# Kernel optimization log

Hardware: AMD Instinct MI355X
Metric: run time of the kernel (lower is better)

The kernel has to match this reference:

```python
import jax, jax.numpy as jnp
import numpy as np

B, NL, L1, D = 16, 12, 197, 768   # batch, num_layers, 1+num_patches, embed_dim
E, K, C, IMG = 4, 3, 21, 224      # num_experts, topk, num_classes, image_size


def setup_inputs() -> dict:
    key = jax.random.key(0)
    k0, k1, k2 = jax.random.split(key, 3)
    features = jax.random.normal(k0, (B, NL, L1, D), jnp.float32)
    gate_W = jax.random.normal(k1, (D, E), jnp.float32) / np.sqrt(D).astype(np.float32)
    gate_b = jnp.zeros((E,), jnp.float32)
    expert_W = jax.random.normal(k2, (E, D, C), jnp.float32) / np.sqrt(D).astype(np.float32)
    expert_b = jnp.zeros((E, C), jnp.float32)
    return dict(features=features, gate_W=gate_W, gate_b=gate_b,
                expert_W=expert_W, expert_b=expert_b)


def reference(features, gate_W, gate_b, expert_W, expert_b):
    cls_tokens = features[:, :, 0, :]          # [B, NL, D]
    feats = features[:, :, 1:, :]              # [B, NL, L, D]
    gate_score = cls_tokens @ gate_W + gate_b  # [B, NL, E]
    gate_prob = jax.nn.softmax(gate_score.transpose(0, 2, 1), axis=-1)  # [B, E, NL]
    # per-expert topk over layers (vectorized over experts)
    topv, topi = jax.lax.top_k(gate_prob, K)   # [B, E, K]
    # gather selected layer feature maps: [B, E, K, L, D]
    gathered = jnp.take_along_axis(feats[:, None], topi[:, :, :, None, None], axis=2)
    w = jax.nn.softmax(topv, axis=-1)          # re-softmax of topk values, [B, E, K]
    mixed = jnp.einsum('bek,bekld->beld', w, gathered)  # [B, E, L, D]
    # expert heads (UPerNet modeled as linear decode + bilinear upsample)
    logits = jnp.einsum('beld,edc->belc', mixed, expert_W) + expert_b[None, :, None, :]
    L = logits.shape[2]
    g = int(np.sqrt(L))                        # 14x14 patch grid
    logits = logits.reshape(B, E, g, g, C).transpose(0, 1, 4, 2, 3)  # [B,E,C,g,g]
    logits = jax.image.resize(logits, (B, E, C, IMG, IMG), method='bilinear')
    return logits.mean(axis=1)                 # mean over experts -> [B, C, IMG, IMG]
```

## Files before the change

### kernel.cpp

```cpp
#include <hip/hip_runtime.h>
#include <math.h>

#define B_ 16
#define NL_ 12
#define L1_ 197
#define D_ 768
#define E_ 4
#define K_ 3
#define C_ 21
#define IMG_ 224
#define LP_ 196
#define NJ_ 84
#define MT_ 52
#define KSTEPS 24
#define KHS 12
#define PROJ_SZ ((size_t)B_ * NL_ * NJ_ * LP_)

typedef __attribute__((ext_vector_type(8))) short short8;
typedef __attribute__((ext_vector_type(4))) float f32x4;
typedef unsigned short ushort_t;

__device__ __forceinline__ ushort_t bf16rne(float x) {
    unsigned u = __float_as_uint(x);
    unsigned r = (u + 0x7FFFu + ((u >> 16) & 1u)) >> 16;
    return (ushort_t)r;
}

__device__ __forceinline__ void select_be(const float* __restrict__ gs, int b, int e,
                                          int idx[3], float w[3]) {
    float p[NL_]; float mx = -1e30f;
    #pragma unroll
    for (int nl = 0; nl < NL_; ++nl) { float v = gs[(b * NL_ + nl) * E_ + e]; p[nl] = v; mx = fmaxf(mx, v); }
    float ss = 0.f;
    #pragma unroll
    for (int nl = 0; nl < NL_; ++nl) { p[nl] = expf(p[nl] - mx); ss += p[nl]; }
    float inv = 1.0f / ss;
    #pragma unroll
    for (int nl = 0; nl < NL_; ++nl) p[nl] *= inv;
    unsigned used = 0; float v[3];
    #pragma unroll
    for (int k = 0; k < 3; ++k) {
        float best = -1.f; int bi = 0;
        #pragma unroll
        for (int nl = 0; nl < NL_; ++nl)
            if (!((used >> nl) & 1u) && p[nl] > best) { best = p[nl]; bi = nl; }
        used |= 1u << bi; idx[k] = bi; v[k] = best;
    }
    float x1 = expf(v[1] - v[0]), x2 = expf(v[2] - v[0]);
    float isw = 1.0f / (1.0f + x1 + x2);
    w[0] = isw; w[1] = x1 * isw; w[2] = x2 * isw;
}

__global__ __launch_bounds__(256) void prep_kernel(
        const float* __restrict__ feat, const float* __restrict__ gW,
        const float* __restrict__ gb, const float* __restrict__ eW,
        ushort_t* __restrict__ WtB, float* __restrict__ gs) {
    int blk = blockIdx.x, t = threadIdx.x;
    if (blk < B_ * NL_) {
        if (t < 64) {
            const float* cls = feat + (size_t)blk * L1_ * D_;
            float a0 = 0.f, a1 = 0.f, a2 = 0.f, a3 = 0.f;
            for (int q = 0; q < D_ / 64; ++q) {
                int d = t + 64 * q;
                float x = cls[d];
                float4 w = *(const float4*)(gW + (size_t)d * E_);
                a0 += x * w.x; a1 += x * w.y; a2 += x * w.z; a3 += x * w.w;
            }
            for (int off = 32; off > 0; off >>= 1) {
                a0 += __shfl_down(a0, off); a1 += __shfl_down(a1, off);
                a2 += __shfl_down(a2, off); a3 += __shfl_down(a3, off);
            }
            if (t == 0) {
                gs[blk * E_ + 0] = a0 + gb[0]; gs[blk * E_ + 1] = a1 + gb[1];
                gs[blk * E_ + 2] = a2 + gb[2]; gs[blk * E_ + 3] = a3 + gb[3];
            }
        }
    } else {
        int j = blk - B_ * NL_;
        if (j < NJ_) {
            int e = j / C_, c = j % C_;
            for (int k = t; k < D_; k += 256)
                WtB[(size_t)j * D_ + k] = bf16rne(eW[((size_t)e * D_ + k) * C_ + c]);
        } else {
            for (int k = t; k < D_; k += 256) WtB[(size_t)j * D_ + k] = 0;
        }
    }
}

__global__ __launch_bounds__(256) void select_kernel(
        const float* __restrict__ gs, int* __restrict__ topi,
        float* __restrict__ wgt, int* __restrict__ flag) {
    __shared__ int sidx[B_ * E_ * 3];
    int t = threadIdx.x;
    if (t < B_ * E_) {
        int b = t >> 2, e = t & 3;
        int idx[3]; float w[3];
        select_be(gs, b, e, idx, w);
        #pragma unroll
        for (int k = 0; k < 3; ++k) {
            topi[t * 3 + k] = idx[k]; wgt[t * 3 + k] = w[k]; sidx[t * 3 + k] = idx[k];
        }
    }
    __syncthreads();
    if (t < B_ * NL_) {
        int b = t / NL_, nl = t % NL_;
        int f = 0;
        #pragma unroll
        for (int ek = 0; ek < 12; ++ek) f |= (sidx[b * 12 + ek] == nl);
        flag[t] = f;
    }
}

#define GLOAD(ks, A0, A1, W0v, W1v) do {                                        \
    int _k0 = (ks) * 32;                                                        \
    if (avalid) { const f32x4* _p = (const f32x4*)(arow_base + _k0);            \
                  A0 = _p[kg * 2]; A1 = _p[kg * 2 + 1]; }                       \
    W0v = *(const short8*)(brow0 + _k0 + kg * 8);                               \
    if (bvalid1) W1v = *(const short8*)(brow1 + _k0 + kg * 8);                  \
} while (0)

#define SSTORE(buf, A0, A1, W0v, W1v) do {                                      \
    short8 _av;                                                                 \
    _Pragma("unroll")                                                           \
    for (int _i = 0; _i < 4; ++_i) {                                            \
        _av[_i]     = (short)bf16rne(A0[_i]);                                   \
        _av[_i + 4] = (short)bf16rne(A1[_i]);                                   \
    }                                                                           \
    Ab[buf][r * 5 + aslotw] = _av;                                              \
    Bb[buf][r * 5 + aslotw] = W0v;                                              \
    if (bvalid1) Bb[buf][(64 + r) * 5 + aslotw] = W1v;                          \
} while (0)

#define COMPUTE(buf) do {                                                       \
    short8 _af = Ab[buf][aidx];                                                 \
    _Pragma("unroll")                                                           \
    for (int _nt = 0; _nt < 6; ++_nt)                                           \
        acc[_nt] = __builtin_amdgcn_mfma_f32_16x16x32_bf16(                     \
            _af, Bb[buf][bidx[_nt]], acc[_nt], 0, 0, 0);                        \
} while (0)

__global__ __launch_bounds__(256, 4) void gemm_kernel(
        const float* __restrict__ feat, const ushort_t* __restrict__ WtB,
        const int* __restrict__ flag, float* __restrict__ proj) {
    int blk = blockIdx.x;
    int kh = blk & 1;
    int tile = (blk >> 1) & 3;
    int bn = blk >> 3;
    if (flag[bn] == 0) return;
    int rows_real = min(MT_, LP_ - tile * MT_);

    __shared__ short8 Ab[2][64 * 5];
    __shared__ short8 Bb[2][96 * 5];

    int t = threadIdx.x;
    int w = t >> 6, lane = t & 63;
    int r = t >> 2, kg = t & 3;
    int aslotw = kg ^ (r & 3);
    bool avalid = r < rows_real;
    bool bvalid1 = t < 128;

    const float* arow_base = feat + ((size_t)bn * L1_ + 1 + tile * MT_ + r) * D_;
    const ushort_t* brow0 = WtB + (size_t)r * D_;
    const ushort_t* brow1 = WtB + (size_t)(64 + r) * D_;

    int arow = w * 16 + (lane & 15);
    int aidx = arow * 5 + ((lane >> 4) ^ (arow & 3));
    int bidx[6];
    #pragma unroll
    for (int nt = 0; nt < 6; ++nt) {
        int jr = nt * 16 + (lane & 15);
        bidx[nt] = jr * 5 + ((lane >> 4) ^ (jr & 3));
    }

    int ks0 = kh * KHS;

    {
        f32x4 fa0 = {0,0,0,0}, fa1 = {0,0,0,0};
        short8 wb0 = (short8)0, wb1 = (short8)0;
        GLOAD(ks0, fa0, fa1, wb0, wb1);
        SSTORE(0, fa0, fa1, wb0, wb1);
    }
    __syncthreads();

    f32x4 acc[6];
    #pragma unroll
    for (int nt = 0; nt < 6; ++nt) acc[nt] = (f32x4)0.0f;

    for (int s = 0; s < KHS; ++s) {
        int cur = s & 1;
        f32x4 fa0 = {0,0,0,0}, fa1 = {0,0,0,0};
        short8 wb0, wb1;
        if (s + 1 < KHS) GLOAD(ks0 + s + 1, fa0, fa1, wb0, wb1);
        COMPUTE(cur);
        if (s + 1 < KHS) SSTORE(cur ^ 1, fa0, fa1, wb0, wb1);
        __syncthreads();
    }

    int lr = w * 16 + ((lane >> 4) << 2);
    int l0 = tile * MT_ + lr;
    if (lr < MT_ && l0 < LP_) {
        float* projh = proj + kh * PROJ_SZ;
        #pragma unroll
        for (int nt = 0; nt < 6; ++nt) {
            int j = nt * 16 + (lane & 15);
            if (j < NJ_)
                *(f32x4*)(projh + ((size_t)bn * NJ_ + j) * LP_ + l0) = acc[nt];
        }
    }
}

__global__ __launch_bounds__(256) void upsample_kernel(
        const float* __restrict__ proj, const int* __restrict__ topi,
        const float* __restrict__ wgt, const float* __restrict__ eb,
        float* __restrict__ out) {
    int bq = blockIdx.x;
    int q = bq & 3;
    int bc = bq >> 2;
    int b = bc / C_, c = bc % C_;
    int t = threadIdx.x;
    __shared__ float s[LP_];
    if (t < LP_) {
        float a = 0.25f * (eb[c] + eb[C_ + c] + eb[2 * C_ + c] + eb[3 * C_ + c]);
        #pragma unroll
        for (int e = 0; e < E_; ++e) {
            int base = (b * E_ + e) * 3;
            #pragma unroll
            for (int k = 0; k < 3; ++k) {
                int nl = topi[base + k];
                float wv = 0.25f * wgt[base + k];
                size_t off = (((size_t)b * NL_ + nl) * NJ_ + e * C_ + c) * LP_ + t;
                a += wv * (proj[off] + proj[off + PROJ_SZ]);
            }
        }
        s[t] = a;
    }
    __syncthreads();
    float4* out4 = (float4*)out + (size_t)bc * IMG_ * (IMG_ / 4);
    for (int i = t; i < 56 * 56; i += 256) {
        int oy = q * 56 + i / 56;
        int ox4 = (i % 56) * 4;
        float fy = (oy + 0.5f) * 0.0625f - 0.5f;
        fy = fminf(fmaxf(fy, 0.0f), 13.0f);
        int y0 = (int)fy;
        float ty = fy - (float)y0;
        int y1 = min(y0 + 1, 13);
        const float* r0 = s + y0 * 14;
        const float* r1 = s + y1 * 14;
        float4 res;
        float* rp = (float*)&res;
        for (int u = 0; u < 4; ++u) {
            int ox = ox4 + u;
            float fx = (ox + 0.5f) * 0.0625f - 0.5f;
            fx = fminf(fmaxf(fx, 0.0f), 13.0f);
            int x0 = (int)fx;
            float tx = fx - (float)x0;
            int x1 = min(x0 + 1, 13);
            float v00 = r0[x0], v01 = r0[x1];
            float v10 = r1[x0], v11 = r1[x1];
            float top = v00 + tx * (v01 - v00);
            float bot = v10 + tx * (v11 - v10);
            rp[u] = top + ty * (bot - top);
        }
        out4[oy * 56 + (i % 56)] = res;
    }
}

extern "C" void kernel_launch(void* const* d_in, const int* in_sizes, int n_in,
                              void* d_out, int out_size, void* d_ws, size_t ws_size,
                              hipStream_t stream) {
    const float* feat = (const float*)d_in[0];
    const float* gW   = (const float*)d_in[1];
    const float* gb   = (const float*)d_in[2];
    const float* eW   = (const float*)d_in[3];
    const float* eb   = (const float*)d_in[4];
    float* out = (float*)d_out;

    float* ws = (float*)d_ws;
    float*    gs   = ws;
    int*      topi = (int*)(ws + 768);
    float*    wgt  = ws + 960;
    int*      flag = (int*)(ws + 1152);
    ushort_t* WtB  = (ushort_t*)(ws + 1536);
    float*    proj = ws + 38400;

    hipLaunchKernelGGL(prep_kernel, dim3(B_ * NL_ + 96), dim3(256), 0, stream,
                       feat, gW, gb, eW, WtB, gs);
    hipLaunchKernelGGL(select_kernel, dim3(1), dim3(256), 0, stream,
                       gs, topi, wgt, flag);
    hipLaunchKernelGGL(gemm_kernel, dim3(B_ * NL_ * 4 * 2), dim3(256), 0, stream,
                       feat, WtB, flag, proj);
    hipLaunchKernelGGL(upsample_kernel, dim3(B_ * C_ * 4), dim3(256), 0, stream,
                       proj, topi, wgt, eb, out);
}
```

Measured before the change: 54.65 us.

## Drop split-K in GEMM, split upsample into eighths, use nontemporal stores

The GEMM kernel no longer splits the K dimension in two. Each block now runs all 24 k-steps and writes a single projection buffer, which halves the GEMM grid and the partial-sum traffic read by the upsample pass. The upsample kernel now splits each output plane into 8 row bands instead of 4, which doubles its grid, and writes output with nontemporal vector stores. The trade-off is fewer GEMM blocks with longer serial loops, which may hurt latency hiding when only flagged layers run, in exchange for less memory traffic and more upsample parallelism.

```diff
diff --git a/kernel.cpp b/kernel.cpp
--- a/kernel.cpp
+++ b/kernel.cpp
@@ -13,8 +13,6 @@
 #define NJ_ 84
 #define MT_ 52
 #define KSTEPS 24
-#define KHS 12
-#define PROJ_SZ ((size_t)B_ * NL_ * NJ_ * LP_)
 
 typedef __attribute__((ext_vector_type(8))) short short8;
 typedef __attribute__((ext_vector_type(4))) float f32x4;
@@ -139,13 +137,12 @@
             _af, Bb[buf][bidx[_nt]], acc[_nt], 0, 0, 0);                        \
 } while (0)
 
-__global__ __launch_bounds__(256, 4) void gemm_kernel(
+__global__ __launch_bounds__(256, 3) void gemm_kernel(
         const float* __restrict__ feat, const ushort_t* __restrict__ WtB,
         const int* __restrict__ flag, float* __restrict__ proj) {
     int blk = blockIdx.x;
-    int kh = blk & 1;
-    int tile = (blk >> 1) & 3;
-    int bn = blk >> 3;
+    int tile = blk & 3;
+    int bn = blk >> 2;
     if (flag[bn] == 0) return;
     int rows_real = min(MT_, LP_ - tile * MT_);
 
@@ -172,12 +169,10 @@
         bidx[nt] = jr * 5 + ((lane >> 4) ^ (jr & 3));
     }
 
-    int ks0 = kh * KHS;
-
     {
         f32x4 fa0 = {0,0,0,0}, fa1 = {0,0,0,0};
         short8 wb0 = (short8)0, wb1 = (short8)0;
-        GLOAD(ks0, fa0, fa1, wb0, wb1);
+        GLOAD(0, fa0, fa1, wb0, wb1);
         SSTORE(0, fa0, fa1, wb0, wb1);
     }
     __syncthreads();
@@ -186,25 +181,24 @@
     #pragma unroll
     for (int nt = 0; nt < 6; ++nt) acc[nt] = (f32x4)0.0f;
 
-    for (int s = 0; s < KHS; ++s) {
+    for (int s = 0; s < KSTEPS; ++s) {
         int cur = s & 1;
         f32x4 fa0 = {0,0,0,0}, fa1 = {0,0,0,0};
         short8 wb0, wb1;
-        if (s + 1 < KHS) GLOAD(ks0 + s + 1, fa0, fa1, wb0, wb1);
+        if (s + 1 < KSTEPS) GLOAD(s + 1, fa0, fa1, wb0, wb1);
         COMPUTE(cur);
-        if (s + 1 < KHS) SSTORE(cur ^ 1, fa0, fa1, wb0, wb1);
+        if (s + 1 < KSTEPS) SSTORE(cur ^ 1, fa0, fa1, wb0, wb1);
         __syncthreads();
     }
 
     int lr = w * 16 + ((lane >> 4) << 2);
     int l0 = tile * MT_ + lr;
     if (lr < MT_ && l0 < LP_) {
-        float* projh = proj + kh * PROJ_SZ;
         #pragma unroll
         for (int nt = 0; nt < 6; ++nt) {
             int j = nt * 16 + (lane & 15);
             if (j < NJ_)
-                *(f32x4*)(projh + ((size_t)bn * NJ_ + j) * LP_ + l0) = acc[nt];
+                *(f32x4*)(proj + ((size_t)bn * NJ_ + j) * LP_ + l0) = acc[nt];
         }
     }
 }
@@ -214,8 +208,8 @@
         const float* __restrict__ wgt, const float* __restrict__ eb,
         float* __restrict__ out) {
     int bq = blockIdx.x;
-    int q = bq & 3;
-    int bc = bq >> 2;
+    int q = bq & 7;
+    int bc = bq >> 3;
     int b = bc / C_, c = bc % C_;
     int t = threadIdx.x;
     __shared__ float s[LP_];
@@ -228,16 +222,15 @@
             for (int k = 0; k < 3; ++k) {
                 int nl = topi[base + k];
                 float wv = 0.25f * wgt[base + k];
-                size_t off = (((size_t)b * NL_ + nl) * NJ_ + e * C_ + c) * LP_ + t;
-                a += wv * (proj[off] + proj[off + PROJ_SZ]);
+                a += wv * proj[(((size_t)b * NL_ + nl) * NJ_ + e * C_ + c) * LP_ + t];
             }
         }
         s[t] = a;
     }
     __syncthreads();
-    float4* out4 = (float4*)out + (size_t)bc * IMG_ * (IMG_ / 4);
-    for (int i = t; i < 56 * 56; i += 256) {
-        int oy = q * 56 + i / 56;
+    f32x4* out4 = (f32x4*)out + (size_t)bc * IMG_ * (IMG_ / 4);
+    for (int i = t; i < 28 * 56; i += 256) {
+        int oy = q * 28 + i / 56;
         int ox4 = (i % 56) * 4;
         float fy = (oy + 0.5f) * 0.0625f - 0.5f;
         fy = fminf(fmaxf(fy, 0.0f), 13.0f);
@@ -246,8 +239,8 @@
         int y1 = min(y0 + 1, 13);
         const float* r0 = s + y0 * 14;
         const float* r1 = s + y1 * 14;
-        float4 res;
-        float* rp = (float*)&res;
+        f32x4 res;
+        #pragma unroll
         for (int u = 0; u < 4; ++u) {
             int ox = ox4 + u;
             float fx = (ox + 0.5f) * 0.0625f - 0.5f;
@@ -259,9 +252,9 @@
             float v10 = r1[x0], v11 = r1[x1];
             float top = v00 + tx * (v01 - v00);
             float bot = v10 + tx * (v11 - v10);
-            rp[u] = top + ty * (bot - top);
-        }
-        out4[oy * 56 + (i % 56)] = res;
+            res[u] = top + ty * (bot - top);
+        }
+        __builtin_nontemporal_store(res, &out4[oy * 56 + (i % 56)]);
     }
 }
 
@@ -287,8 +280,8 @@
                        feat, gW, gb, eW, WtB, gs);
     hipLaunchKernelGGL(select_kernel, dim3(1), dim3(256), 0, stream,
                        gs, topi, wgt, flag);
-    hipLaunchKernelGGL(gemm_kernel, dim3(B_ * NL_ * 4 * 2), dim3(256), 0, stream,
+    hipLaunchKernelGGL(gemm_kernel, dim3(B_ * NL_ * 4), dim3(256), 0, stream,
                        feat, WtB, flag, proj);
-    hipLaunchKernelGGL(upsample_kernel, dim3(B_ * C_ * 4), dim3(256), 0, stream,
+    hipLaunchKernelGGL(upsample_kernel, dim3(B_ * C_ * 8), dim3(256), 0, stream,
                        proj, topi, wgt, eb, out);
 }
```

Result: faster. 52.60 us (-3.7%).
